# Performance work log

Measured on AMD Instinct MI355X. Metric: run time of the kernel, lower is better.

Reference implementation:

```python
import jax, jax.numpy as jnp
import numpy as np

BS, N, DEG = 2, 16384, 16
NE = N * DEG          # 262144 edges
D = 128               # node/edge feature dim
S = 4                 # number of completed blocks
EPS = 1e-6


def mlp(x, W1, b1, W2, b2):
    # MLP(in, hidden=128, out, act=SiLU, layer_norm=False)
    return jax.nn.silu(x @ W1 + b1) @ W2 + b2


def rms_norm(x, w):
    return x * jax.lax.rsqrt(jnp.mean(x * x, axis=-1, keepdims=True) + EPS) * w


def setup_inputs() -> dict:
    key = jax.random.key(0)
    ks = jax.random.split(key, 14)
    f32 = jnp.float32
    sc = 0.05
    return {
        "V": jax.random.normal(ks[0], (BS, N, D), f32),
        "E": jax.random.normal(ks[1], (BS, NE, D), f32),
        "blocks": jax.random.normal(ks[2], (S, BS, N, D), f32),
        "We1": jax.random.normal(ks[3], (3 * D, D), f32) * sc,
        "be1": jnp.zeros((D,), f32),
        "We2": jax.random.normal(ks[4], (D, D), f32) * sc,
        "be2": jnp.zeros((D,), f32),
        "Wn1": jax.random.normal(ks[5], (2 * D, D), f32) * sc,
        "bn1": jnp.zeros((D,), f32),
        "Wn2": jax.random.normal(ks[6], (D, D), f32) * sc,
        "bn2": jnp.zeros((D,), f32),
        "w_attn": jax.random.normal(ks[7], (D,), f32) * sc,
        "rms_w": jnp.ones((D,), f32),
        "edges": jax.random.randint(ks[8], (BS, NE, 2), 0, N, jnp.int32),
    }


def reference(V, E, blocks, We1, be1, We2, be2, Wn1, bn1, Wn2, bn2,
              w_attn, rms_w, edges):
    # ---- GNN layer: edge gather -> edge MLP -> scatter_mean -> node MLP ----
    senders = jnp.take_along_axis(V, edges[..., 0][:, :, None], axis=1)    # [b,E,D]
    receivers = jnp.take_along_axis(V, edges[..., 1][:, :, None], axis=1)  # [b,E,D]
    edge_inpt = jnp.concatenate([senders, receivers, E], axis=-1)          # [b,E,3D]
    edge_emb = mlp(edge_inpt, We1, be1, We2, be2)                          # [b,E,D]
    e0, e1 = jnp.split(edge_emb, 2, axis=-1)                               # [b,E,D/2] each

    def seg_mean(vals, idx):
        s = jax.ops.segment_sum(vals, idx, num_segments=N)
        c = jax.ops.segment_sum(jnp.ones(idx.shape, vals.dtype), idx,
                                num_segments=N)
        return s / jnp.maximum(c, 1.0)[:, None]

    m0 = jax.vmap(seg_mean)(e0, edges[..., 0])   # [b,N,D/2]
    m1 = jax.vmap(seg_mean)(e1, edges[..., 1])   # [b,N,D/2]
    node_inpt = jnp.concatenate([V, m0, m1], axis=-1)                      # [b,N,2D]
    node_emb = mlp(node_inpt, Wn1, bn1, Wn2, bn2)                          # [b,N,D]

    # ---- block_attn_res: depth-wise attention over stacked blocks ----
    Vs = jnp.concatenate([blocks, node_emb[None]], axis=0)                 # [S+1,b,N,D]
    K = rms_norm(Vs, rms_w)
    logits = jnp.einsum('d,sbnd->sbn', w_attn, K)
    alpha = jax.nn.softmax(logits, axis=0)
    h = jnp.einsum('sbn,sbnd->bnd', alpha, Vs)                             # [b,N,D]
    return h
```

## Files before the change

kernel.cpp:

```cpp
#include <hip/hip_runtime.h>
#include <hip/hip_bf16.h>

#define D 128
#define NNODES 16384
#define NEDGES 262144
#define NBATCH 2
#define TE 64

typedef __attribute__((ext_vector_type(8))) short bf16x8;
typedef __attribute__((ext_vector_type(4))) float f32x4;

__device__ __forceinline__ unsigned short f2bf(float f) {
    unsigned int u = __float_as_uint(f);
    unsigned int r = (u + 0x7fffu + ((u >> 16) & 1u)) >> 16;
    return (unsigned short)r;
}

__device__ __forceinline__ unsigned int pk2bf(float lo, float hi) {
    return (unsigned int)f2bf(lo) | ((unsigned int)f2bf(hi) << 16);
}

__device__ __forceinline__ float bf2f(unsigned short u) {
    return __uint_as_float(((unsigned int)u) << 16);
}

__device__ __forceinline__ bf16x8 pack8(f32x4 a, f32x4 b) {
    unsigned int w0 = pk2bf(a[0], a[1]);
    unsigned int w1 = pk2bf(a[2], a[3]);
    unsigned int w2 = pk2bf(b[0], b[1]);
    unsigned int w3 = pk2bf(b[2], b[3]);
    typedef __attribute__((ext_vector_type(4))) unsigned int u32x4;
    u32x4 u; u.x = w0; u.y = w1; u.z = w2; u.w = w3;
    return __builtin_bit_cast(bf16x8, u);
}

__device__ __forceinline__ void atomic_pk(unsigned int* p, unsigned int v) {
    asm volatile("global_atomic_pk_add_bf16 %0, %1, off" :: "v"(p), "v"(v) : "memory");
}

__global__ __launch_bounds__(256)
void prep_weights(const float* __restrict__ We1, const float* __restrict__ We2,
                  const float* __restrict__ Wn1, const float* __restrict__ Wn2,
                  unsigned short* __restrict__ w)
{
    int id = blockIdx.x * 256 + threadIdx.x;
    if (id < 16384) {
        int e = id & 7, l = (id >> 3) & 63, nblk = (id >> 9) & 7, ks = id >> 12;
        int k = 256 + ks * 32 + ((l >> 4) & 3) * 8 + e;
        int col = nblk * 16 + (l & 15);
        w[id] = f2bf(We1[k * 128 + col]);
    } else if (id < 32768) {
        int i2 = id - 16384;
        int e = i2 & 7, l = (i2 >> 3) & 63, nblk = (i2 >> 9) & 7, ks = i2 >> 12;
        int k = ks * 32 + ((l >> 4) & 3) * 8 + e;
        int col = nblk * 16 + (l & 15);
        w[id] = f2bf(We2[k * 128 + col]);
    } else if (id < 65536) {
        int i3 = id - 32768;
        int j = i3 >> 7, k = i3 & 127;
        int row = (j < 128) ? k : (128 + k);
        w[id] = f2bf(We1[row * 128 + (j & 127)]);
    } else if (id < 98304) {
        int i4 = id - 65536;
        int n = i4 >> 8, k = i4 & 255;
        w[id] = f2bf(Wn1[k * 128 + n]);
    } else {
        int i5 = id - 98304;
        int n = i5 >> 7, k = i5 & 127;
        w[id] = f2bf(Wn2[k * 128 + n]);
    }
}

__global__ __launch_bounds__(256)
void partial_kernel(const float* __restrict__ V, const unsigned short* __restrict__ wp,
                    unsigned short* __restrict__ P)
{
    __shared__ unsigned short smem[64 * 136];
    const int t = threadIdx.x, lane = t & 63, wave = t >> 6;
    const int l15 = lane & 15, l4 = lane >> 4;
    const long long r0 = (long long)blockIdx.x * 64;

    for (int i = t; i < 64 * 32; i += 256) {
        int c4 = i & 31, r = i >> 5;
        float4 v = *(const float4*)(V + (r0 + r) * 128 + c4 * 4);
        uint2 p; p.x = pk2bf(v.x, v.y); p.y = pk2bf(v.z, v.w);
        *(uint2*)(&smem[r * 136 + c4 * 4]) = p;
    }
    __syncthreads();

    const int j0 = wave * 64;
    f32x4 acc[4][4] = {};
    const unsigned short* bb0 = wp + (j0 + l15) * 128 + l4 * 8;
    #pragma unroll
    for (int ks = 0; ks < 4; ++ks) {
        bf16x8 bb[4];
        #pragma unroll
        for (int n = 0; n < 4; ++n)
            bb[n] = *(const bf16x8*)(bb0 + n * 16 * 128 + ks * 32);
        #pragma unroll
        for (int mq = 0; mq < 4; ++mq) {
            bf16x8 a = *(const bf16x8*)(&smem[(mq * 16 + l15) * 136 + l4 * 8 + ks * 32]);
            #pragma unroll
            for (int n = 0; n < 4; ++n)
                acc[mq][n] = __builtin_amdgcn_mfma_f32_16x16x32_bf16(a, bb[n], acc[mq][n], 0, 0, 0);
        }
    }
    #pragma unroll
    for (int mq = 0; mq < 4; ++mq) {
        #pragma unroll
        for (int n = 0; n < 4; ++n) {
            #pragma unroll
            for (int i = 0; i < 4; ++i) {
                int row = mq * 16 + l4 * 4 + i;
                int col = j0 + n * 16 + l15;
                P[(r0 + row) * 256 + col] = f2bf(acc[mq][n][i]);
            }
        }
    }
}

__global__ __launch_bounds__(256)
void edge_kernel(const float* __restrict__ E, const int* __restrict__ edges,
                 const unsigned short* __restrict__ P,
                 const unsigned short* __restrict__ w1ef, const float* __restrict__ be1,
                 const unsigned short* __restrict__ w2f,
                 unsigned short* __restrict__ us_m0, unsigned short* __restrict__ us_m1,
                 float* __restrict__ c0, float* __restrict__ c1)
{
    __shared__ unsigned short Hbuf[TE * 136];

    const int t    = threadIdx.x;
    const int lane = t & 63;
    const int wave = t >> 6;
    const int wr   = wave >> 1;
    const int wc   = wave & 1;
    const int l15  = lane & 15;
    const int l4   = lane >> 4;

    const long long eflat0 = (long long)blockIdx.x * TE;
    const int b  = (int)(eflat0 / NEDGES);
    const long long nb0 = (long long)b * NNODES;

    if (t < TE) {
        int2 e2 = *(const int2*)(edges + (eflat0 + t) * 2);
        atomicAdd(&c0[nb0 + e2.x], 1.f);
        atomicAdd(&c1[nb0 + e2.y], 1.f);
    }

    f32x4 acc[2][4] = {};
    {
        const float* er0 = E + (eflat0 + wr * 32 + l15) * D + l4 * 8;
        #pragma unroll
        for (int ks = 0; ks < 4; ++ks) {
            f32x4 xa0 = *(const f32x4*)(er0 + ks * 32);
            f32x4 xb0 = *(const f32x4*)(er0 + ks * 32 + 4);
            f32x4 xa1 = *(const f32x4*)(er0 + 16 * D + ks * 32);
            f32x4 xb1 = *(const f32x4*)(er0 + 16 * D + ks * 32 + 4);
            bf16x8 a0 = pack8(xa0, xb0);
            bf16x8 a1 = pack8(xa1, xb1);
            #pragma unroll
            for (int n = 0; n < 4; ++n) {
                bf16x8 bb = *(const bf16x8*)(w1ef + (((ks * 8 + wc * 4 + n) * 64 + lane) << 3));
                acc[0][n] = __builtin_amdgcn_mfma_f32_16x16x32_bf16(a0, bb, acc[0][n], 0, 0, 0);
                acc[1][n] = __builtin_amdgcn_mfma_f32_16x16x32_bf16(a1, bb, acc[1][n], 0, 0, 0);
            }
        }
    }

    int nd0[2][4], nd1[2][4];
    #pragma unroll
    for (int m = 0; m < 2; ++m) {
        #pragma unroll
        for (int i = 0; i < 4; ++i) {
            int row = wr * 32 + m * 16 + l4 * 4 + i;
            int2 e2 = *(const int2*)(edges + (eflat0 + row) * 2);
            nd0[m][i] = e2.x;
            nd1[m][i] = e2.y;
        }
    }

    #pragma unroll
    for (int n = 0; n < 4; ++n) {
        int col = wc * 64 + n * 16 + l15;
        float bias = be1[col];
        #pragma unroll
        for (int m = 0; m < 2; ++m) {
            #pragma unroll
            for (int i = 0; i < 4; ++i) {
                int row = wr * 32 + m * 16 + l4 * 4 + i;
                float a = acc[m][n][i] + bias
                        + bf2f(P[(nb0 + nd0[m][i]) * 256 + col])
                        + bf2f(P[(nb0 + nd1[m][i]) * 256 + 128 + col]);
                Hbuf[row * 136 + col] = f2bf(a / (1.f + __expf(-a)));
            }
        }
    }
    __syncthreads();

    f32x4 acc2[2][4] = {};
    {
        const unsigned short* hrow = &Hbuf[(wr * 32 + l15) * 136 + l4 * 8];
        #pragma unroll
        for (int ks = 0; ks < 4; ++ks) {
            bf16x8 a0 = *(const bf16x8*)(hrow + ks * 32);
            bf16x8 a1 = *(const bf16x8*)(hrow + 16 * 136 + ks * 32);
            #pragma unroll
            for (int n = 0; n < 4; ++n) {
                bf16x8 bb = *(const bf16x8*)(w2f + (((ks * 8 + wc * 4 + n) * 64 + lane) << 3));
                acc2[0][n] = __builtin_amdgcn_mfma_f32_16x16x32_bf16(a0, bb, acc2[0][n], 0, 0, 0);
                acc2[1][n] = __builtin_amdgcn_mfma_f32_16x16x32_bf16(a1, bb, acc2[1][n], 0, 0, 0);
            }
        }
    }

    {
        unsigned short* dst_arr = wc ? us_m1 : us_m0;
        #pragma unroll
        for (int n = 0; n < 4; ++n) {
            int colh = n * 16 + l15;
            #pragma unroll
            for (int m = 0; m < 2; ++m) {
                #pragma unroll
                for (int i = 0; i < 4; ++i) {
                    int node = wc ? nd1[m][i] : nd0[m][i];
                    float v  = acc2[m][n][i];
                    float vn = __shfl_xor(v, 1);
                    if (!(lane & 1)) {
                        atomic_pk((unsigned int*)(dst_arr + (nb0 + node) * 64 + colh),
                                  pk2bf(v, vn));
                    }
                }
            }
        }
    }
}

__global__ __launch_bounds__(256)
void node_kernel(const float* __restrict__ V,
                 const unsigned short* __restrict__ m0, const unsigned short* __restrict__ m1,
                 const float* __restrict__ c0, const float* __restrict__ c1,
                 const float* __restrict__ be2,
                 const unsigned short* __restrict__ wn1t, const float* __restrict__ bn1,
                 const unsigned short* __restrict__ wn2t, const float* __restrict__ bn2,
                 float* __restrict__ node_emb)
{
    __shared__ unsigned short smem[TE * 264];

    const int t    = threadIdx.x;
    const int lane = t & 63;
    const int wave = t >> 6;
    const int wr   = wave >> 1;
    const int wc   = wave & 1;
    const int l15  = lane & 15;
    const int l4   = lane >> 4;

    const long long nflat0 = (long long)blockIdx.x * TE;

    for (int i = t; i < TE * 48; i += 256) {
        int n  = i / 48;
        int c4 = i - n * 48;
        long long node = nflat0 + n;
        if (c4 < 32) {
            float4 v = *(const float4*)(V + node * 128 + c4 * 4);
            uint2 p; p.x = pk2bf(v.x, v.y); p.y = pk2bf(v.z, v.w);
            *(uint2*)(&smem[n * 264 + c4 * 4]) = p;
        } else {
            int dir = (c4 >= 40);
            int j = c4 - 32 - dir * 8;
            const unsigned short* src = dir ? m1 : m0;
            float cnt = (dir ? c1 : c0)[node];
            float inv = 1.f / fmaxf(cnt, 1.f);
            float bon = (cnt >= 1.f) ? 1.f : 0.f;
            uint4 raw = *(const uint4*)(src + node * 64 + j * 8);
            const float* bb = be2 + dir * 64 + j * 8;
            unsigned int rr[4] = {raw.x, raw.y, raw.z, raw.w};
            unsigned int o[4];
            #pragma unroll
            for (int q = 0; q < 4; ++q) {
                float lo = bf2f((unsigned short)(rr[q] & 0xffffu)) * inv + bb[2 * q] * bon;
                float hi = bf2f((unsigned short)(rr[q] >> 16)) * inv + bb[2 * q + 1] * bon;
                o[q] = pk2bf(lo, hi);
            }
            uint4 st; st.x = o[0]; st.y = o[1]; st.z = o[2]; st.w = o[3];
            *(uint4*)(&smem[n * 264 + 128 + dir * 64 + j * 8]) = st;
        }
    }
    __syncthreads();

    f32x4 acc[2][4] = {};
    {
        const unsigned short* arow = &smem[(wr * 32 + l15) * 264 + l4 * 8];
        const unsigned short* bb0  = wn1t + (wc * 64 + l15) * 256 + l4 * 8;
        for (int ks = 0; ks < 8; ++ks) {
            bf16x8 a0 = *(const bf16x8*)(arow + ks * 32);
            bf16x8 a1 = *(const bf16x8*)(arow + 16 * 264 + ks * 32);
            #pragma unroll
            for (int n = 0; n < 4; ++n) {
                bf16x8 bb = *(const bf16x8*)(bb0 + n * 16 * 256 + ks * 32);
                acc[0][n] = __builtin_amdgcn_mfma_f32_16x16x32_bf16(a0, bb, acc[0][n], 0, 0, 0);
                acc[1][n] = __builtin_amdgcn_mfma_f32_16x16x32_bf16(a1, bb, acc[1][n], 0, 0, 0);
            }
        }
    }
    __syncthreads();

    #pragma unroll
    for (int n = 0; n < 4; ++n) {
        int col = wc * 64 + n * 16 + l15;
        float bias = bn1[col];
        #pragma unroll
        for (int m = 0; m < 2; ++m) {
            #pragma unroll
            for (int i = 0; i < 4; ++i) {
                int row = wr * 32 + m * 16 + l4 * 4 + i;
                float a = acc[m][n][i] + bias;
                smem[row * 136 + col] = f2bf(a / (1.f + __expf(-a)));
            }
        }
    }
    __syncthreads();

    f32x4 acc2[2][4] = {};
    {
        const unsigned short* hrow = &smem[(wr * 32 + l15) * 136 + l4 * 8];
        const unsigned short* bb0  = wn2t + (wc * 64 + l15) * 128 + l4 * 8;
        #pragma unroll
        for (int ks = 0; ks < 4; ++ks) {
            bf16x8 a0 = *(const bf16x8*)(hrow + ks * 32);
            bf16x8 a1 = *(const bf16x8*)(hrow + 16 * 136 + ks * 32);
            #pragma unroll
            for (int n = 0; n < 4; ++n) {
                bf16x8 bb = *(const bf16x8*)(bb0 + n * 16 * 128 + ks * 32);
                acc2[0][n] = __builtin_amdgcn_mfma_f32_16x16x32_bf16(a0, bb, acc2[0][n], 0, 0, 0);
                acc2[1][n] = __builtin_amdgcn_mfma_f32_16x16x32_bf16(a1, bb, acc2[1][n], 0, 0, 0);
            }
        }
    }

    #pragma unroll
    for (int n = 0; n < 4; ++n) {
        int col = wc * 64 + n * 16 + l15;
        float bias = bn2[col];
        #pragma unroll
        for (int m = 0; m < 2; ++m) {
            #pragma unroll
            for (int i = 0; i < 4; ++i) {
                long long row = nflat0 + wr * 32 + m * 16 + l4 * 4 + i;
                node_emb[row * 128 + col] = acc2[m][n][i] + bias;
            }
        }
    }
}

__global__ __launch_bounds__(256)
void attn_kernel(const float* __restrict__ blocks, const float* __restrict__ node_emb,
                 const float* __restrict__ w_attn, const float* __restrict__ rms_w,
                 float* __restrict__ out)
{
    const int t    = threadIdx.x;
    const int wave = t >> 6;
    const int lane = t & 63;
    const long long node = (long long)blockIdx.x * 4 + wave;
    const int d0 = lane * 2;

    float2 wa = *(const float2*)(w_attn + d0);
    float2 rw = *(const float2*)(rms_w + d0);

    float xs[5][2];
    float lg[5];
    #pragma unroll
    for (int s = 0; s < 5; ++s) {
        const float* src = (s < 4)
            ? (blocks + ((long long)s * NBATCH * NNODES + node) * 128)
            : (node_emb + node * 128);
        float2 x = *(const float2*)(src + d0);
        xs[s][0] = x.x; xs[s][1] = x.y;
        float ss = x.x * x.x + x.y * x.y;
        float wv = wa.x * rw.x * x.x + wa.y * rw.y * x.y;
        #pragma unroll
        for (int m = 1; m < 64; m <<= 1) {
            ss += __shfl_xor(ss, m);
            wv += __shfl_xor(wv, m);
        }
        lg[s] = wv * rsqrtf(ss * (1.f / 128.f) + 1e-6f);
    }

    float mx = lg[0];
    #pragma unroll
    for (int s = 1; s < 5; ++s) mx = fmaxf(mx, lg[s]);
    float ex[5], sum = 0.f;
    #pragma unroll
    for (int s = 0; s < 5; ++s) { ex[s] = __expf(lg[s] - mx); sum += ex[s]; }
    float inv = 1.f / sum;

    float h0 = 0.f, h1 = 0.f;
    #pragma unroll
    for (int s = 0; s < 5; ++s) {
        float a = ex[s] * inv;
        h0 = fmaf(a, xs[s][0], h0);
        h1 = fmaf(a, xs[s][1], h1);
    }
    *(float2*)(out + node * 128 + d0) = make_float2(h0, h1);
}

extern "C" void kernel_launch(void* const* d_in, const int* in_sizes, int n_in,
                              void* d_out, int out_size, void* d_ws, size_t ws_size,
                              hipStream_t stream)
{
    const float* V      = (const float*)d_in[0];
    const float* E      = (const float*)d_in[1];
    const float* blocks = (const float*)d_in[2];
    const float* We1    = (const float*)d_in[3];
    const float* be1    = (const float*)d_in[4];
    const float* We2    = (const float*)d_in[5];
    const float* be2    = (const float*)d_in[6];
    const float* Wn1    = (const float*)d_in[7];
    const float* bn1    = (const float*)d_in[8];
    const float* Wn2    = (const float*)d_in[9];
    const float* bn2    = (const float*)d_in[10];
    const float* w_attn = (const float*)d_in[11];
    const float* rms_w  = (const float*)d_in[12];
    const int*   edges  = (const int*)d_in[13];
    float* out = (float*)d_out;

    unsigned short* us_m0 = (unsigned short*)d_ws;
    unsigned short* us_m1 = us_m0 + 2097152;
    float* c0       = (float*)(us_m1 + 2097152);
    float* c1       = c0 + 32768;
    float* node_emb = c1 + 32768;
    unsigned short* wbf = (unsigned short*)(node_emb + 4194304);
    unsigned short* w1ef = wbf;
    unsigned short* w2f  = wbf + 16384;
    unsigned short* wp   = wbf + 32768;
    unsigned short* wn1t = wbf + 65536;
    unsigned short* wn2t = wbf + 98304;
    unsigned short* P    = wbf + 114688;

    (void)hipMemsetAsync(d_ws, 0, (size_t)(2097152 * 2 * 2 + 32768 * 2 * 4), stream);

    prep_weights<<<448, 256, 0, stream>>>(We1, We2, Wn1, Wn2, wbf);

    partial_kernel<<<(NBATCH * NNODES) / 64, 256, 0, stream>>>(V, wp, P);

    edge_kernel<<<(NBATCH * NEDGES) / TE, 256, 0, stream>>>(
        E, edges, P, w1ef, be1, w2f, us_m0, us_m1, c0, c1);

    node_kernel<<<(NBATCH * NNODES) / TE, 256, 0, stream>>>(
        V, us_m0, us_m1, c0, c1, be2, wn1t, bn1, wn2t, bn2, node_emb);

    attn_kernel<<<(NBATCH * NNODES) / 4, 256, 0, stream>>>(
        blocks, node_emb, w_attn, rms_w, out);
}
```

Before: 376.5 us.

## Permute P columns for vectorized gathers and double edge tile to 512 threads

The partial projection table P is written with a permuted column layout, so each lane's four columns are contiguous. The edge kernel can then fetch sender and receiver partials with one 8-byte load per edge instead of four scalar bf16 loads. The edge tile also grows from 64 to 128 edges with 512-thread blocks, and node_kernel is pinned to its old 64-node tile. This cuts gather instruction count and per-block overhead, at the cost of larger blocks that may lower occupancy.

```diff
diff --git a/kernel.cpp b/kernel.cpp
--- a/kernel.cpp
+++ b/kernel.cpp
@@ -5,7 +5,7 @@
 #define NNODES 16384
 #define NEDGES 262144
 #define NBATCH 2
-#define TE 64
+#define TE 128
 
 typedef __attribute__((ext_vector_type(8))) short bf16x8;
 typedef __attribute__((ext_vector_type(4))) float f32x4;
@@ -22,6 +22,13 @@
 
 __device__ __forceinline__ float bf2f(unsigned short u) {
     return __uint_as_float(((unsigned int)u) << 16);
+}
+
+__device__ __forceinline__ float bflo(unsigned int u) {
+    return __uint_as_float(u << 16);
+}
+__device__ __forceinline__ float bfhi(unsigned int u) {
+    return __uint_as_float(u & 0xffff0000u);
 }
 
 __device__ __forceinline__ bf16x8 pack8(f32x4 a, f32x4 b) {
@@ -105,6 +112,7 @@
                 acc[mq][n] = __builtin_amdgcn_mfma_f32_16x16x32_bf16(a, bb[n], acc[mq][n], 0, 0, 0);
         }
     }
+    const int pbase = (wave >> 1) * 128 + (wave & 1) * 64 + l15 * 4;
     #pragma unroll
     for (int mq = 0; mq < 4; ++mq) {
         #pragma unroll
@@ -112,14 +120,13 @@
             #pragma unroll
             for (int i = 0; i < 4; ++i) {
                 int row = mq * 16 + l4 * 4 + i;
-                int col = j0 + n * 16 + l15;
-                P[(r0 + row) * 256 + col] = f2bf(acc[mq][n][i]);
-            }
-        }
-    }
-}
-
-__global__ __launch_bounds__(256)
+                P[(r0 + row) * 256 + pbase + n] = f2bf(acc[mq][n][i]);
+            }
+        }
+    }
+}
+
+__global__ __launch_bounds__(512)
 void edge_kernel(const float* __restrict__ E, const int* __restrict__ edges,
                  const unsigned short* __restrict__ P,
                  const unsigned short* __restrict__ w1ef, const float* __restrict__ be1,
@@ -179,19 +186,34 @@
         }
     }
 
-    #pragma unroll
-    for (int n = 0; n < 4; ++n) {
-        int col = wc * 64 + n * 16 + l15;
-        float bias = be1[col];
-        #pragma unroll
-        for (int m = 0; m < 2; ++m) {
-            #pragma unroll
-            for (int i = 0; i < 4; ++i) {
-                int row = wr * 32 + m * 16 + l4 * 4 + i;
-                float a = acc[m][n][i] + bias
-                        + bf2f(P[(nb0 + nd0[m][i]) * 256 + col])
-                        + bf2f(P[(nb0 + nd1[m][i]) * 256 + 128 + col]);
-                Hbuf[row * 136 + col] = f2bf(a / (1.f + __expf(-a)));
+    const unsigned short* Pb = P + nb0 * 256;
+    const unsigned int wcl = wc * 64 + l15 * 4;
+    uint2 su[2][4], ru[2][4];
+    #pragma unroll
+    for (int m = 0; m < 2; ++m) {
+        #pragma unroll
+        for (int i = 0; i < 4; ++i) {
+            su[m][i] = *(const uint2*)(Pb + (unsigned)nd0[m][i] * 256u + wcl);
+            ru[m][i] = *(const uint2*)(Pb + (unsigned)nd1[m][i] * 256u + 128u + wcl);
+        }
+    }
+
+    float bia[4];
+    #pragma unroll
+    for (int n = 0; n < 4; ++n) bia[n] = be1[wc * 64 + n * 16 + l15];
+    #pragma unroll
+    for (int m = 0; m < 2; ++m) {
+        #pragma unroll
+        for (int i = 0; i < 4; ++i) {
+            int row = wr * 32 + m * 16 + l4 * 4 + i;
+            float ps[4] = { bflo(su[m][i].x), bfhi(su[m][i].x),
+                            bflo(su[m][i].y), bfhi(su[m][i].y) };
+            float pr[4] = { bflo(ru[m][i].x), bfhi(ru[m][i].x),
+                            bflo(ru[m][i].y), bfhi(ru[m][i].y) };
+            #pragma unroll
+            for (int n = 0; n < 4; ++n) {
+                float a = acc[m][n][i] + bia[n] + ps[n] + pr[n];
+                Hbuf[row * 136 + wc * 64 + n * 16 + l15] = f2bf(a / (1.f + __expf(-a)));
             }
         }
     }
@@ -244,7 +266,7 @@
                  const unsigned short* __restrict__ wn2t, const float* __restrict__ bn2,
                  float* __restrict__ node_emb)
 {
-    __shared__ unsigned short smem[TE * 264];
+    __shared__ unsigned short smem[64 * 264];
 
     const int t    = threadIdx.x;
     const int lane = t & 63;
@@ -254,9 +276,9 @@
     const int l15  = lane & 15;
     const int l4   = lane >> 4;
 
-    const long long nflat0 = (long long)blockIdx.x * TE;
-
-    for (int i = t; i < TE * 48; i += 256) {
+    const long long nflat0 = (long long)blockIdx.x * 64;
+
+    for (int i = t; i < 64 * 48; i += 256) {
         int n  = i / 48;
         int c4 = i - n * 48;
         long long node = nflat0 + n;
@@ -277,8 +299,8 @@
             unsigned int o[4];
             #pragma unroll
             for (int q = 0; q < 4; ++q) {
-                float lo = bf2f((unsigned short)(rr[q] & 0xffffu)) * inv + bb[2 * q] * bon;
-                float hi = bf2f((unsigned short)(rr[q] >> 16)) * inv + bb[2 * q + 1] * bon;
+                float lo = bflo(rr[q]) * inv + bb[2 * q] * bon;
+                float hi = bfhi(rr[q]) * inv + bb[2 * q + 1] * bon;
                 o[q] = pk2bf(lo, hi);
             }
             uint4 st; st.x = o[0]; st.y = o[1]; st.z = o[2]; st.w = o[3];
@@ -442,10 +464,10 @@
 
     partial_kernel<<<(NBATCH * NNODES) / 64, 256, 0, stream>>>(V, wp, P);
 
-    edge_kernel<<<(NBATCH * NEDGES) / TE, 256, 0, stream>>>(
+    edge_kernel<<<(NBATCH * NEDGES) / TE, 512, 0, stream>>>(
         E, edges, P, w1ef, be1, w2f, us_m0, us_m1, c0, c1);
 
-    node_kernel<<<(NBATCH * NNODES) / TE, 256, 0, stream>>>(
+    node_kernel<<<(NBATCH * NNODES) / 64, 256, 0, stream>>>(
         V, us_m0, us_m1, c0, c1, be2, wn1t, bn1, wn2t, bn2, node_emb);
 
     attn_kernel<<<(NBATCH * NNODES) / 4, 256, 0, stream>>>(
```

Measured after the change: 364.9 us. 1.03x faster.
